# Kernel tuning notes

Measured on AMD Instinct MI355X. Metric: run time of the kernel, lower is better.

Reference implementation:

```python
import jax, jax.numpy as jnp
import numpy as np

B, T, C = 2, 2048, 1024
NH = 16

def setup_inputs() -> dict:
    key = jax.random.key(0)
    ks = jax.random.split(key, 5)
    s = 0.02
    return {
        "x": jax.random.normal(ks[0], (B, T, C), dtype=jnp.float32),
        "w_attn": jax.random.normal(ks[1], (C, 3 * C), dtype=jnp.float32) * s,
        "b_attn": jax.random.normal(ks[2], (3 * C,), dtype=jnp.float32) * s,
        "w_proj": jax.random.normal(ks[3], (C, C), dtype=jnp.float32) * s,
        "b_proj": jax.random.normal(ks[4], (C,), dtype=jnp.float32) * s,
        "n_heads": NH,
    }

def reference(x, w_attn, b_attn, w_proj, b_proj, n_heads):
    Bx, Tx, Cx = x.shape
    hd = Cx // n_heads
    qkv = x @ w_attn + b_attn                      # [B,T,3C]
    q, k, v = jnp.split(qkv, 3, axis=-1)
    # [B,T,H,hd] -> [B,H,T,hd]
    q = q.reshape(Bx, Tx, n_heads, hd).transpose(0, 2, 1, 3)
    k = k.reshape(Bx, Tx, n_heads, hd).transpose(0, 2, 1, 3)
    v = v.reshape(Bx, Tx, n_heads, hd).transpose(0, 2, 1, 3)
    scale = 1.0 / np.sqrt(hd).astype(np.float32)
    att = jnp.einsum('bhqd,bhkd->bhqk', q, k) * scale   # [B,H,T,T]
    causal = jnp.tril(jnp.ones((Tx, Tx), dtype=bool))
    att = jnp.where(causal[None, None], att, -jnp.inf)
    att = jax.nn.softmax(att, axis=-1)
    y = jnp.einsum('bhqk,bhkd->bhqd', att, v)            # [B,H,T,hd]
    y = y.transpose(0, 2, 1, 3).reshape(Bx, Tx, Cx)
    return y @ w_proj + b_proj
```

## Files before the change

kernel.cpp:

```cpp
#include <hip/hip_runtime.h>

typedef __bf16 bf16x8 __attribute__((ext_vector_type(8)));
typedef __bf16 bf16x4 __attribute__((ext_vector_type(4)));
typedef float  f32x4  __attribute__((ext_vector_type(4)));

#define MFMA_BF16(a, b, c) __builtin_amdgcn_mfma_f32_16x16x32_bf16((a), (b), (c), 0, 0, 0)
#define NEG_INF (-1e30f)
#define SCL 0.18033688f

__device__ __forceinline__ void gld16(const void* g, void* l) {
  __builtin_amdgcn_global_load_lds(
      (const __attribute__((address_space(1))) void*)g,
      (__attribute__((address_space(3))) void*)l, 16, 0, 0);
}

__global__ void cast_f32_bf16(const float* __restrict__ in,
                              __bf16* __restrict__ out, int n) {
  int i = (blockIdx.x * 256 + threadIdx.x) * 8;
  if (i >= n) return;
  float4 a = *(const float4*)&in[i];
  float4 b = *(const float4*)&in[i + 4];
  bf16x8 v;
  v[0] = (__bf16)a.x; v[1] = (__bf16)a.y; v[2] = (__bf16)a.z; v[3] = (__bf16)a.w;
  v[4] = (__bf16)b.x; v[5] = (__bf16)b.y; v[6] = (__bf16)b.z; v[7] = (__bf16)b.w;
  *(bf16x8*)&out[i] = v;
}

__global__ void transpose_f32_bf16(const float* __restrict__ in,
                                   __bf16* __restrict__ out, int R, int C) {
  __shared__ float t[32][33];
  int tx = threadIdx.x & 31, ty = threadIdx.x >> 5;
  int x = blockIdx.x * 32 + tx;
  int y0 = blockIdx.y * 32 + ty;
#pragma unroll
  for (int i = 0; i < 4; ++i)
    t[ty + 8 * i][tx] = in[(size_t)(y0 + 8 * i) * C + x];
  __syncthreads();
  int x2 = blockIdx.y * 32 + tx;
#pragma unroll
  for (int i = 0; i < 4; ++i)
    out[(size_t)(blockIdx.x * 32 + ty + 8 * i) * R + x2] = (__bf16)t[tx][ty + 8 * i];
}

#define BN 128
#define BK 64

template <int BMT, typename TC>
__global__ __launch_bounds__(256) void gemm_bt_bias(
    const __bf16* __restrict__ A, const __bf16* __restrict__ Bt,
    const float* __restrict__ bias, TC* __restrict__ Cmat,
    int M, int N, int K) {
  constexpr int NI = BMT / 32;
  __shared__ __align__(16) __bf16 As[BMT * BK];
  __shared__ __align__(16) __bf16 Bs[BN * BK];
  int tid = threadIdx.x;
  int wave = tid >> 6, lane = tid & 63;
  int l16 = lane & 15, quad = lane >> 4;
  int wm = wave >> 1, wn = wave & 1;
  int m0 = blockIdx.y * BMT, n0 = blockIdx.x * BN;

  f32x4 acc[NI][4];
#pragma unroll
  for (int i = 0; i < NI; ++i)
#pragma unroll
    for (int j = 0; j < 4; ++j) acc[i][j] = (f32x4){0.f, 0.f, 0.f, 0.f};

  int row = tid >> 3;
  int kc = ((tid & 7) ^ ((tid >> 3) & 7)) * 8;
  int xr = (l16 & 7) * 8;

  for (int k0 = 0; k0 < K; k0 += BK) {
#pragma unroll
    for (int i = 0; i < NI; ++i)
      gld16(&A[(size_t)(m0 + row + i * 32) * K + k0 + kc],
            (char*)As + (i * 256 + wave * 64) * 16);
#pragma unroll
    for (int j = 0; j < 4; ++j)
      gld16(&Bt[(size_t)(n0 + row + j * 32) * K + k0 + kc],
            (char*)Bs + (j * 256 + wave * 64) * 16);
    __syncthreads();
#pragma unroll
    for (int ks = 0; ks < 2; ++ks) {
      bf16x8 af[NI], bfr[4];
#pragma unroll
      for (int i = 0; i < NI; ++i)
        af[i] = *(const bf16x8*)&As[(wm * (BMT / 2) + i * 16 + l16) * BK +
                                    ((ks * 32 + quad * 8) ^ xr)];
#pragma unroll
      for (int j = 0; j < 4; ++j)
        bfr[j] = *(const bf16x8*)&Bs[(wn * 64 + j * 16 + l16) * BK +
                                     ((ks * 32 + quad * 8) ^ xr)];
#pragma unroll
      for (int i = 0; i < NI; ++i)
#pragma unroll
        for (int j = 0; j < 4; ++j) acc[i][j] = MFMA_BF16(af[i], bfr[j], acc[i][j]);
    }
    __syncthreads();
  }
#pragma unroll
  for (int i = 0; i < NI; ++i) {
#pragma unroll
    for (int j = 0; j < 4; ++j) {
      int col = n0 + wn * 64 + j * 16 + l16;
      float bv = bias[col];
#pragma unroll
      for (int r = 0; r < 4; ++r) {
        int rw = m0 + wm * (BMT / 2) + i * 16 + quad * 4 + r;
        Cmat[(size_t)rw * N + col] = (TC)(acc[i][j][r] + bv);
      }
    }
  }
}

#define BARX do { asm volatile("" ::: "memory"); __builtin_amdgcn_s_barrier(); \
                  asm volatile("" ::: "memory"); } while (0)
#define WLGKM do { asm volatile("s_waitcnt lgkmcnt(0)" ::: "memory"); \
                   __builtin_amdgcn_sched_barrier(0); } while (0)
#define WVM4 asm volatile("s_waitcnt vmcnt(4)" ::: "memory")
#define STA8(SBUF, SKS, T) do { \
    gld16(srcA1 + (size_t)(T) * 64 + (SKS) * 32, (char*)&As[SBUF][SKS][0] + tid * 16); \
    gld16(srcA2 + (size_t)(T) * 64 + (SKS) * 32, (char*)&As[SBUF][SKS][0] + tid * 16 + 8192); \
  } while (0)
#define STB8(SBUF, SKS, T) do { \
    gld16(srcB1 + (size_t)(T) * 64 + (SKS) * 32, (char*)&Bs[SBUF][SKS][0] + tid * 16); \
    gld16(srcB2 + (size_t)(T) * 64 + (SKS) * 32, (char*)&Bs[SBUF][SKS][0] + tid * 16 + 8192); \
  } while (0)
#define LDA4(CBUF, CKS, MQ) do { \
    const __bf16* p_ = &As[CBUF][CKS][(wm * 128 + (MQ) * 64 + l16) * 32 + xrd]; \
    af[0] = *(const bf16x8*)(p_);        af[1] = *(const bf16x8*)(p_ + 512); \
    af[2] = *(const bf16x8*)(p_ + 1024); af[3] = *(const bf16x8*)(p_ + 1536); \
  } while (0)
#define LDB3(CBUF, CKS) do { \
    const __bf16* p_ = &Bs[CBUF][CKS][(wn * 48 + l16) * 32 + xrd]; \
    bfr[0] = *(const bf16x8*)(p_);       bfr[1] = *(const bf16x8*)(p_ + 512); \
    bfr[2] = *(const bf16x8*)(p_ + 1024); \
  } while (0)
#define MM12(MQ) do { \
    __builtin_amdgcn_s_setprio(1); \
    _Pragma("unroll") for (int mi_ = 0; mi_ < 4; ++mi_) \
    _Pragma("unroll") for (int nj_ = 0; nj_ < 3; ++nj_) \
      acc[(MQ) * 4 + mi_][nj_] = MFMA_BF16(af[mi_], bfr[nj_], acc[(MQ) * 4 + mi_][nj_]); \
    __builtin_amdgcn_s_setprio(0); \
  } while (0)

__global__ __launch_bounds__(512, 2) void gemm_qkv_8ph(
    const __bf16* __restrict__ A, const __bf16* __restrict__ Bt,
    const float* __restrict__ bias, __bf16* __restrict__ qkv,
    __bf16* __restrict__ vt) {
  constexpr int GK = 1024, GN = 3072, NT = 16;
  __shared__ __align__(16) __bf16 As[2][2][256 * 32];
  __shared__ __align__(16) __bf16 Bs[2][2][256 * 32];
  const int tid = threadIdx.x;
  const int wave = tid >> 6, lane = tid & 63;
  const int l16 = lane & 15, quad = lane >> 4;
  const int wm = wave >> 2, wn = wave & 3;
  const int m0 = blockIdx.y * 256, n0 = blockIdx.x * 192;

  const int row0 = tid >> 2;
  const int kc = (((tid & 3) ^ ((row0 >> 1) & 3)) * 8);
  const int xrd = (quad ^ ((l16 >> 1) & 3)) * 8;

  const __bf16* srcA1 = A + (size_t)(m0 + row0) * GK + kc;
  const __bf16* srcA2 = srcA1 + (size_t)128 * GK;
  const __bf16* srcB1 = Bt + (size_t)(n0 + row0) * GK + kc;
  const int br2 = (row0 + 128 < 192) ? row0 + 128 : 191;
  const __bf16* srcB2 = Bt + (size_t)(n0 + br2) * GK + kc;

  f32x4 acc[8][3];
#pragma unroll
  for (int m = 0; m < 8; ++m)
#pragma unroll
    for (int n = 0; n < 3; ++n) acc[m][n] = (f32x4){0.f, 0.f, 0.f, 0.f};

  STA8(0, 0, 0); STB8(0, 0, 0);
  STA8(0, 1, 0); STB8(0, 1, 0);
  STA8(1, 0, 1); STB8(1, 0, 1);
  WVM4;
  BARX;

  bf16x8 af[4], bfr[3];
#pragma unroll 1
  for (int i = 0; i < NT / 2; ++i) {
    const int v = 2 * i + 1;
    const int t2 = (2 * i + 2 < NT) ? 2 * i + 2 : NT - 1;
    const int t3 = (2 * i + 3 < NT) ? 2 * i + 3 : NT - 1;
    LDA4(0, 0, 0); LDB3(0, 0); STA8(1, 1, v);
    BARX; WLGKM; MM12(0); BARX;
    LDA4(0, 0, 1); STB8(1, 1, v);
    BARX; WLGKM; MM12(1); BARX;
    LDA4(0, 1, 0); LDB3(0, 1); STA8(0, 0, t2);
    BARX; WLGKM; MM12(0); BARX;
    LDA4(0, 1, 1); STB8(0, 0, t2);
    BARX; WLGKM; MM12(1); WVM4; BARX;
    LDA4(1, 0, 0); LDB3(1, 0); STA8(0, 1, t2);
    BARX; WLGKM; MM12(0); BARX;
    LDA4(1, 0, 1); STB8(0, 1, t2);
    BARX; WLGKM; MM12(1); BARX;
    LDA4(1, 1, 0); LDB3(1, 1); STA8(1, 0, t3);
    BARX; WLGKM; MM12(0); BARX;
    LDA4(1, 1, 1); STB8(1, 0, t3);
    BARX; WLGKM; MM12(1); WVM4; BARX;
  }

#pragma unroll
  for (int n = 0; n < 3; ++n) {
    const int c0 = n0 + wn * 48 + n * 16;
    const int col = c0 + l16;
    const float bv = bias[col];
    if (c0 < 2048) {
#pragma unroll
      for (int m = 0; m < 8; ++m) {
        const int rw = m0 + wm * 128 + m * 16 + quad * 4;
#pragma unroll
        for (int r = 0; r < 4; ++r)
          qkv[(size_t)(rw + r) * GN + col] = (__bf16)(acc[m][n][r] + bv);
      }
    } else {
      const int h = (col - 2048) >> 6, d = col & 63;
#pragma unroll
      for (int m = 0; m < 8; ++m) {
        const int t0 = m0 + wm * 128 + m * 16 + quad * 4;
        const int b = t0 >> 11, tt = t0 & 2047;
        bf16x4 pb;
#pragma unroll
        for (int r = 0; r < 4; ++r) pb[r] = (__bf16)(acc[m][n][r] + bv);
        *(bf16x4*)&vt[(size_t)((b * 16 + h) * 64 + d) * 2048 + tt] = pb;
      }
    }
  }
}

__global__ __launch_bounds__(256, 3) void attn_causal(
    const __bf16* __restrict__ qkv, const __bf16* __restrict__ vt,
    __bf16* __restrict__ y) {
  __shared__ __align__(16) __bf16 Kb[2][64 * 64];
  __shared__ __align__(16) __bf16 Vb[2][64 * 64];
  __shared__ __align__(16) __bf16 Ps[4][16 * 72];
  const int tid = threadIdx.x;
  const int wave = tid >> 6, lane = tid & 63;
  const int l16 = lane & 15, quad = lane >> 4;
  const int bh = blockIdx.x;
  const int b = bh >> 4, h = bh & 15;
  const int RS = 3072;
  const int qt = 31 - (int)blockIdx.y;

  const int row0 = tid >> 3;
  const int kcs = ((tid & 7) ^ ((tid >> 3) & 7)) * 8;
  const int xr = (l16 & 7) * 8;
  const __bf16* kbase = qkv + (size_t)(b * 2048) * RS + 1024 + h * 64 + kcs;
  const __bf16* vbase = vt + (size_t)(bh * 64) * 2048 + kcs;

  int qrow = b * 2048 + qt * 64 + wave * 16 + l16;
  const __bf16* qbase = qkv + (size_t)qrow * RS + h * 64;
  bf16x8 qf0 = *(const bf16x8*)(qbase + quad * 8);
  bf16x8 qf1 = *(const bf16x8*)(qbase + 32 + quad * 8);

  float l4[4] = {0.f, 0.f, 0.f, 0.f};
  f32x4 o[4];
#pragma unroll
  for (int j = 0; j < 4; ++j) o[j] = (f32x4){0.f, 0.f, 0.f, 0.f};

#pragma unroll
  for (int i = 0; i < 2; ++i) {
    gld16(kbase + (size_t)(row0 + 32 * i) * RS,
          (char*)Kb[0] + (i * 256 + tid) * 16);
    gld16(vbase + (size_t)(row0 + 32 * i) * 2048,
          (char*)Vb[0] + (i * 256 + tid) * 16);
  }
  __syncthreads();

  for (int kt = 0; kt <= qt; ++kt) {
    const int cur = kt & 1;
    if (kt < qt) {
#pragma unroll
      for (int i = 0; i < 2; ++i) {
        gld16(kbase + (size_t)((kt + 1) * 64 + row0 + 32 * i) * RS,
              (char*)Kb[cur ^ 1] + (i * 256 + tid) * 16);
        gld16(vbase + (size_t)(row0 + 32 * i) * 2048 + (kt + 1) * 64,
              (char*)Vb[cur ^ 1] + (i * 256 + tid) * 16);
      }
    }

    f32x4 s[4];
#pragma unroll
    for (int j = 0; j < 4; ++j) s[j] = (f32x4){0.f, 0.f, 0.f, 0.f};
    __builtin_amdgcn_s_setprio(1);
#pragma unroll
    for (int j = 0; j < 4; ++j) {
      bf16x8 kf0 = *(const bf16x8*)&Kb[cur][(j * 16 + l16) * 64 + ((quad * 8) ^ xr)];
      bf16x8 kf1 = *(const bf16x8*)&Kb[cur][(j * 16 + l16) * 64 + ((32 + quad * 8) ^ xr)];
      s[j] = MFMA_BF16(kf0, qf0, s[j]);
      s[j] = MFMA_BF16(kf1, qf1, s[j]);
    }
    __builtin_amdgcn_s_setprio(0);

    if (kt == qt) {
      int qg = wave * 16 + l16;
#pragma unroll
      for (int j = 0; j < 4; ++j)
#pragma unroll
        for (int r = 0; r < 4; ++r)
          if (j * 16 + quad * 4 + r > qg) s[j][r] = NEG_INF;
    }

#pragma unroll
    for (int j = 0; j < 4; ++j) {
      bf16x4 pb;
#pragma unroll
      for (int r = 0; r < 4; ++r) {
        float p = __builtin_amdgcn_exp2f(s[j][r] * SCL);
        l4[j] += p;
        pb[r] = (__bf16)p;
      }
      *(bf16x4*)&Ps[wave][l16 * 72 + j * 16 + quad * 4] = pb;
    }

    __builtin_amdgcn_s_setprio(1);
#pragma unroll
    for (int ks = 0; ks < 2; ++ks) {
      bf16x8 pf = *(const bf16x8*)&Ps[wave][l16 * 72 + ks * 32 + quad * 8];
#pragma unroll
      for (int j = 0; j < 4; ++j) {
        bf16x8 vf = *(const bf16x8*)&Vb[cur][(j * 16 + l16) * 64 +
                                            ((ks * 32 + quad * 8) ^ xr)];
        o[j] = MFMA_BF16(pf, vf, o[j]);
      }
    }
    __builtin_amdgcn_s_setprio(0);
    __syncthreads();
  }

  float lred = (l4[0] + l4[1]) + (l4[2] + l4[3]);
  lred += __shfl_xor(lred, 16);
  lred += __shfl_xor(lred, 32);
  int orow = b * 2048 + qt * 64 + wave * 16 + quad * 4;
#pragma unroll
  for (int r = 0; r < 4; ++r) {
    float inv = 1.f / __shfl(lred, quad * 4 + r);
#pragma unroll
    for (int j = 0; j < 4; ++j)
      y[(size_t)(orow + r) * 1024 + h * 64 + j * 16 + l16] = (__bf16)(o[j][r] * inv);
  }
}

extern "C" void kernel_launch(void* const* d_in, const int* in_sizes, int n_in,
                              void* d_out, int out_size, void* d_ws, size_t ws_size,
                              hipStream_t stream) {
  (void)in_sizes; (void)n_in; (void)out_size; (void)ws_size;
  const float* x      = (const float*)d_in[0];
  const float* w_attn = (const float*)d_in[1];
  const float* b_attn = (const float*)d_in[2];
  const float* w_proj = (const float*)d_in[3];
  const float* b_proj = (const float*)d_in[4];
  float* out = (float*)d_out;

  __bf16* wt_attn = (__bf16*)d_ws;
  __bf16* wt_proj = wt_attn + (size_t)3072 * 1024;
  __bf16* qkv     = wt_proj + (size_t)1024 * 1024;
  __bf16* ybuf    = qkv + (size_t)4096 * 3072;
  __bf16* vtbuf   = ybuf + (size_t)4096 * 1024;

  cast_f32_bf16<<<4096 * 1024 / 2048, 256, 0, stream>>>(x, ybuf, 4096 * 1024);

  transpose_f32_bf16<<<dim3(3072 / 32, 1024 / 32), 256, 0, stream>>>(w_attn, wt_attn, 1024, 3072);
  transpose_f32_bf16<<<dim3(1024 / 32, 1024 / 32), 256, 0, stream>>>(w_proj, wt_proj, 1024, 1024);

  gemm_qkv_8ph<<<dim3(3072 / 192, 4096 / 256), 512, 0, stream>>>(
      ybuf, wt_attn, b_attn, qkv, vtbuf);

  attn_causal<<<dim3(32, 32), 256, 0, stream>>>(qkv, vtbuf, ybuf);

  gemm_bt_bias<64, float><<<dim3(1024 / BN, 4096 / 64), 256, 0, stream>>>(
      ybuf, wt_proj, b_proj, out, 4096, 1024, 1024);
}
```

Baseline: 179.3 us.

## Switch attention to 32x32 MFMA with register-resident P via permlane swap

The causal attention kernel is rebuilt around 32x32x16 bf16 MFMAs. Each wave now owns 32 query rows, so a block has 2 waves (128 threads) instead of 4. The softmax probabilities are packed to bf16 with v_cvt_pk and rearranged across lane halves with v_permlane32_swap, then fed straight into the PV MFMA as operands. This removes the per-wave shared-memory staging buffer for P and its LDS round trip, and simplifies the final row-sum reduction. In exchange each block has fewer waves to hide latency, each thread holds more accumulator registers, and the inline asm depends on gfx950 lane-swap semantics being correct.

```diff
diff --git a/kernel.cpp b/kernel.cpp
--- a/kernel.cpp
+++ b/kernel.cpp
@@ -3,8 +3,11 @@
 typedef __bf16 bf16x8 __attribute__((ext_vector_type(8)));
 typedef __bf16 bf16x4 __attribute__((ext_vector_type(4)));
 typedef float  f32x4  __attribute__((ext_vector_type(4)));
+typedef float  f32x16 __attribute__((ext_vector_type(16)));
+typedef unsigned int u32;
 
 #define MFMA_BF16(a, b, c) __builtin_amdgcn_mfma_f32_16x16x32_bf16((a), (b), (c), 0, 0, 0)
+#define MFMA32(a, b, c) __builtin_amdgcn_mfma_f32_32x32x16_bf16((a), (b), (c), 0, 0, 0)
 #define NEG_INF (-1e30f)
 #define SCL 0.18033688f
 
@@ -230,116 +233,140 @@
   }
 }
 
-__global__ __launch_bounds__(256, 3) void attn_causal(
+#define CVTPK(D, LO, HI) \
+  asm("v_cvt_pk_bf16_f32 %0, %1, %2" : "=v"(D) : "v"(LO), "v"(HI))
+#define SWAP32(DST, SRC) \
+  asm("v_permlane32_swap_b32 %0, %1" : "+v"(DST), "+v"(SRC))
+
+__device__ __forceinline__ bf16x8 mk8(u32 a, u32 b, u32 c, u32 d) {
+  union { u32 u[4]; bf16x8 h; } x;
+  x.u[0] = a; x.u[1] = b; x.u[2] = c; x.u[3] = d;
+  return x.h;
+}
+
+__global__ __launch_bounds__(128, 3) void attn_causal(
     const __bf16* __restrict__ qkv, const __bf16* __restrict__ vt,
     __bf16* __restrict__ y) {
   __shared__ __align__(16) __bf16 Kb[2][64 * 64];
   __shared__ __align__(16) __bf16 Vb[2][64 * 64];
-  __shared__ __align__(16) __bf16 Ps[4][16 * 72];
   const int tid = threadIdx.x;
   const int wave = tid >> 6, lane = tid & 63;
-  const int l16 = lane & 15, quad = lane >> 4;
+  const int l32 = lane & 31, hi = lane >> 5;
   const int bh = blockIdx.x;
   const int b = bh >> 4, h = bh & 15;
   const int RS = 3072;
   const int qt = 31 - (int)blockIdx.y;
 
-  const int row0 = tid >> 3;
-  const int kcs = ((tid & 7) ^ ((tid >> 3) & 7)) * 8;
-  const int xr = (l16 & 7) * 8;
+  const int row8 = tid >> 3;
+  const int kcs = ((tid & 7) ^ (row8 & 7)) * 8;
   const __bf16* kbase = qkv + (size_t)(b * 2048) * RS + 1024 + h * 64 + kcs;
   const __bf16* vbase = vt + (size_t)(bh * 64) * 2048 + kcs;
 
-  int qrow = b * 2048 + qt * 64 + wave * 16 + l16;
-  const __bf16* qbase = qkv + (size_t)qrow * RS + h * 64;
-  bf16x8 qf0 = *(const bf16x8*)(qbase + quad * 8);
-  bf16x8 qf1 = *(const bf16x8*)(qbase + 32 + quad * 8);
+  const __bf16* qp = qkv + (size_t)(b * 2048 + qt * 64 + wave * 32 + l32) * RS +
+                     h * 64 + hi * 8;
+  bf16x8 qf[4];
+#pragma unroll
+  for (int kc = 0; kc < 4; ++kc) qf[kc] = *(const bf16x8*)(qp + kc * 16);
 
   float l4[4] = {0.f, 0.f, 0.f, 0.f};
-  f32x4 o[4];
-#pragma unroll
-  for (int j = 0; j < 4; ++j) o[j] = (f32x4){0.f, 0.f, 0.f, 0.f};
-
-#pragma unroll
-  for (int i = 0; i < 2; ++i) {
-    gld16(kbase + (size_t)(row0 + 32 * i) * RS,
-          (char*)Kb[0] + (i * 256 + tid) * 16);
-    gld16(vbase + (size_t)(row0 + 32 * i) * 2048,
-          (char*)Vb[0] + (i * 256 + tid) * 16);
+  f32x16 o0, o1;
+#pragma unroll
+  for (int r = 0; r < 16; ++r) { o0[r] = 0.f; o1[r] = 0.f; }
+
+#pragma unroll
+  for (int i = 0; i < 4; ++i) {
+    gld16(kbase + (size_t)(i * 16 + row8) * RS, (char*)Kb[0] + (i * 128 + tid) * 16);
+    gld16(vbase + (size_t)(i * 16 + row8) * 2048, (char*)Vb[0] + (i * 128 + tid) * 16);
   }
   __syncthreads();
 
+  const int xr7 = l32 & 7;
   for (int kt = 0; kt <= qt; ++kt) {
     const int cur = kt & 1;
     if (kt < qt) {
 #pragma unroll
-      for (int i = 0; i < 2; ++i) {
-        gld16(kbase + (size_t)((kt + 1) * 64 + row0 + 32 * i) * RS,
-              (char*)Kb[cur ^ 1] + (i * 256 + tid) * 16);
-        gld16(vbase + (size_t)(row0 + 32 * i) * 2048 + (kt + 1) * 64,
-              (char*)Vb[cur ^ 1] + (i * 256 + tid) * 16);
-      }
-    }
-
-    f32x4 s[4];
-#pragma unroll
-    for (int j = 0; j < 4; ++j) s[j] = (f32x4){0.f, 0.f, 0.f, 0.f};
+      for (int i = 0; i < 4; ++i) {
+        gld16(kbase + (size_t)((kt + 1) * 64 + i * 16 + row8) * RS,
+              (char*)Kb[cur ^ 1] + (i * 128 + tid) * 16);
+        gld16(vbase + (size_t)(i * 16 + row8) * 2048 + (kt + 1) * 64,
+              (char*)Vb[cur ^ 1] + (i * 128 + tid) * 16);
+      }
+    }
+
+    f32x16 c0, c1;
+#pragma unroll
+    for (int r = 0; r < 16; ++r) { c0[r] = 0.f; c1[r] = 0.f; }
     __builtin_amdgcn_s_setprio(1);
 #pragma unroll
-    for (int j = 0; j < 4; ++j) {
-      bf16x8 kf0 = *(const bf16x8*)&Kb[cur][(j * 16 + l16) * 64 + ((quad * 8) ^ xr)];
-      bf16x8 kf1 = *(const bf16x8*)&Kb[cur][(j * 16 + l16) * 64 + ((32 + quad * 8) ^ xr)];
-      s[j] = MFMA_BF16(kf0, qf0, s[j]);
-      s[j] = MFMA_BF16(kf1, qf1, s[j]);
+    for (int kc = 0; kc < 4; ++kc) {
+      const int sw = ((kc * 2 + hi) ^ xr7) << 3;
+      bf16x8 kf0 = *(const bf16x8*)&Kb[cur][l32 * 64 + sw];
+      bf16x8 kf1 = *(const bf16x8*)&Kb[cur][(32 + l32) * 64 + sw];
+      c0 = MFMA32(kf0, qf[kc], c0);
+      c1 = MFMA32(kf1, qf[kc], c1);
     }
     __builtin_amdgcn_s_setprio(0);
 
     if (kt == qt) {
-      int qg = wave * 16 + l16;
-#pragma unroll
-      for (int j = 0; j < 4; ++j)
-#pragma unroll
-        for (int r = 0; r < 4; ++r)
-          if (j * 16 + quad * 4 + r > qg) s[j][r] = NEG_INF;
-    }
-
-#pragma unroll
-    for (int j = 0; j < 4; ++j) {
-      bf16x4 pb;
-#pragma unroll
-      for (int r = 0; r < 4; ++r) {
-        float p = __builtin_amdgcn_exp2f(s[j][r] * SCL);
-        l4[j] += p;
-        pb[r] = (__bf16)p;
-      }
-      *(bf16x4*)&Ps[wave][l16 * 72 + j * 16 + quad * 4] = pb;
+      const int qloc = wave * 32 + l32;
+#pragma unroll
+      for (int r = 0; r < 16; ++r) {
+        const int kl = (r & 3) + 8 * (r >> 2) + 4 * hi;
+        if (kl > qloc) c0[r] = NEG_INF;
+        if (32 + kl > qloc) c1[r] = NEG_INF;
+      }
+    }
+
+    bf16x8 pb[4];
+#pragma unroll
+    for (int kb = 0; kb < 2; ++kb) {
+      float pv[16];
+#pragma unroll
+      for (int r = 0; r < 16; ++r) {
+        const float sv = (kb ? c1[r] : c0[r]);
+        pv[r] = __builtin_amdgcn_exp2f(sv * SCL);
+        l4[r & 3] += pv[r];
+      }
+      u32 a0, a1, b0, b1;
+      CVTPK(a0, pv[0], pv[1]);   CVTPK(a1, pv[2], pv[3]);
+      CVTPK(b0, pv[4], pv[5]);   CVTPK(b1, pv[6], pv[7]);
+      SWAP32(a0, b0); SWAP32(a1, b1);
+      pb[kb * 2 + 0] = mk8(a0, a1, b0, b1);
+      CVTPK(a0, pv[8], pv[9]);   CVTPK(a1, pv[10], pv[11]);
+      CVTPK(b0, pv[12], pv[13]); CVTPK(b1, pv[14], pv[15]);
+      SWAP32(a0, b0); SWAP32(a1, b1);
+      pb[kb * 2 + 1] = mk8(a0, a1, b0, b1);
     }
 
     __builtin_amdgcn_s_setprio(1);
 #pragma unroll
-    for (int ks = 0; ks < 2; ++ks) {
-      bf16x8 pf = *(const bf16x8*)&Ps[wave][l16 * 72 + ks * 32 + quad * 8];
-#pragma unroll
-      for (int j = 0; j < 4; ++j) {
-        bf16x8 vf = *(const bf16x8*)&Vb[cur][(j * 16 + l16) * 64 +
-                                            ((ks * 32 + quad * 8) ^ xr)];
-        o[j] = MFMA_BF16(pf, vf, o[j]);
-      }
+    for (int kc = 0; kc < 4; ++kc) {
+      const int sw = ((kc * 2 + hi) ^ xr7) << 3;
+      bf16x8 vf0 = *(const bf16x8*)&Vb[cur][l32 * 64 + sw];
+      bf16x8 vf1 = *(const bf16x8*)&Vb[cur][(32 + l32) * 64 + sw];
+      o0 = MFMA32(vf0, pb[kc], o0);
+      o1 = MFMA32(vf1, pb[kc], o1);
     }
     __builtin_amdgcn_s_setprio(0);
     __syncthreads();
   }
 
   float lred = (l4[0] + l4[1]) + (l4[2] + l4[3]);
-  lred += __shfl_xor(lred, 16);
   lred += __shfl_xor(lred, 32);
-  int orow = b * 2048 + qt * 64 + wave * 16 + quad * 4;
-#pragma unroll
-  for (int r = 0; r < 4; ++r) {
-    float inv = 1.f / __shfl(lred, quad * 4 + r);
-#pragma unroll
-    for (int j = 0; j < 4; ++j)
-      y[(size_t)(orow + r) * 1024 + h * 64 + j * 16 + l16] = (__bf16)(o[j][r] * inv);
+  const float inv = 1.f / lred;
+
+  const int orow = b * 2048 + qt * 64 + wave * 32 + l32;
+  __bf16* yb = y + (size_t)orow * 1024 + h * 64 + hi * 4;
+#pragma unroll
+  for (int db = 0; db < 2; ++db) {
+#pragma unroll
+    for (int g = 0; g < 4; ++g) {
+      bf16x4 w;
+#pragma unroll
+      for (int j = 0; j < 4; ++j)
+        w[j] = (__bf16)((db ? o1[g * 4 + j] : o0[g * 4 + j]) * inv);
+      *(bf16x4*)&yb[db * 32 + g * 8] = w;
+    }
   }
 }
 
@@ -368,7 +395,7 @@
   gemm_qkv_8ph<<<dim3(3072 / 192, 4096 / 256), 512, 0, stream>>>(
       ybuf, wt_attn, b_attn, qkv, vtbuf);
 
-  attn_causal<<<dim3(32, 32), 256, 0, stream>>>(qkv, vtbuf, ybuf);
+  attn_causal<<<dim3(32, 32), 128, 0, stream>>>(qkv, vtbuf, ybuf);
 
   gemm_bt_bias<64, float><<<dim3(1024 / BN, 4096 / 64), 256, 0, stream>>>(
       ybuf, wt_proj, b_proj, out, 4096, 1024, 1024);
```

Result: slower. 184.7 us (+3.0%).
